# Performance work log

Hardware: AMD Instinct MI355X
Metric: run time of the kernel (lower is better)

## Reference

```python
import jax, jax.numpy as jnp
import numpy as np

DECAY = 0.99
EPSILON = 1e-05
CODEBOOK_SIZE = 1024
DIM = 128


def setup_inputs() -> dict:
    key = jax.random.key(0)
    k1, k2, k3, k4 = jax.random.split(key, 4)
    x = jax.random.normal(k1, (8, 8192, DIM), dtype=jnp.float32)
    embed = jax.random.normal(k2, (CODEBOOK_SIZE, DIM), dtype=jnp.float32)
    cluster_size = jax.random.uniform(k3, (CODEBOOK_SIZE,), dtype=jnp.float32)
    embed_avg = jax.random.normal(k4, (CODEBOOK_SIZE, DIM), dtype=jnp.float32)
    return {"x": x, "embed": embed, "cluster_size": cluster_size, "embed_avg": embed_avg}


def reference(x, embed, cluster_size, embed_avg):
    shape = x.shape
    flat = x.reshape(-1, shape[-1])  # [N, dim]

    # quantize: negative squared euclidean distance, argmax == nearest code
    dist = -(jnp.sum(flat * flat, axis=1, keepdims=True)
             - 2.0 * flat @ embed.T
             + jnp.sum(embed * embed, axis=1)[None, :])  # [N, K]
    embed_ind = jnp.argmax(dist, axis=-1)  # [N]

    quantize = embed[embed_ind].reshape(shape)            # dequantize
    embed_ind_out = embed_ind.reshape(shape[:-1])

    # training-time EMA updates (one-hot expressed as segment_sum)
    batch_cluster_size = jax.ops.segment_sum(
        jnp.ones_like(embed_ind, dtype=flat.dtype), embed_ind,
        num_segments=CODEBOOK_SIZE)                       # == one_hot.sum(0)
    new_cluster_size = cluster_size * DECAY + (1.0 - DECAY) * batch_cluster_size

    embed_sum = jax.ops.segment_sum(flat, embed_ind,
                                    num_segments=CODEBOOK_SIZE)  # == (x.T @ one_hot).T
    new_embed_avg = embed_avg * DECAY + (1.0 - DECAY) * embed_sum

    total = new_cluster_size.sum()
    smoothed = (new_cluster_size + EPSILON) / (total + CODEBOOK_SIZE * EPSILON)
    smoothed_counts = smoothed * total
    new_embed = new_embed_avg / smoothed_counts[:, None]

    return quantize, embed_ind_out, new_cluster_size, new_embed_avg, new_embed
```

## Files before the change

kernel.cpp:

```cpp
#include <hip/hip_runtime.h>
#include <math.h>

#define DIM 128
#define KCODES 1024
#define NROWS 65536

typedef short bf16x8 __attribute__((ext_vector_type(8)));
typedef float f32x4 __attribute__((ext_vector_type(4)));

#define WS_COUNTS 0
#define WS_ESUM   1024
#define WS_IOFF   132096
#define WS_TOTAL  133120
#define WS_ENORM2 133124
#define WS_EBF    134148
#define WS_WIN    461828
#define WS_SORTED 527364
#define WS_SCODE  592900

#define OFF_Q   0
#define OFF_IND 8388608
#define OFF_NCS 8454144
#define OFF_NEA 8455168
#define OFF_NE  8586240

#define LDST 136

static __device__ __forceinline__ unsigned short f2bf(float f) {
    unsigned u = __float_as_uint(f);
    unsigned r = (u + 0x7FFFu + ((u >> 16) & 1u)) >> 16;
    return (unsigned short)r;
}

__global__ __launch_bounds__(64) void k_prep(const float* __restrict__ embed,
                                             unsigned short* __restrict__ ebf,
                                             float* __restrict__ en2,
                                             float* __restrict__ counts,
                                             float* __restrict__ esum) {
    int k = blockIdx.x;
    int l = threadIdx.x;
    if (l == 0) counts[k] = 0.0f;
    *(float2*)&esum[(size_t)k * DIM + l * 2] = (float2){0.0f, 0.0f};
    float2 v = *(const float2*)&embed[(size_t)k * DIM + l * 2];
    ushort2 b;
    b.x = f2bf(v.x);
    b.y = f2bf(v.y);
    *(ushort2*)&ebf[k * DIM + l * 2] = b;
    float s = v.x * v.x + v.y * v.y;
    #pragma unroll
    for (int off = 32; off; off >>= 1) s += __shfl_xor(s, off);
    if (l == 0) en2[k] = 512.0f - 0.5f * s;
}

__global__ __launch_bounds__(256, 2) void k_fused(const float* __restrict__ x,
                                                  const float* __restrict__ embed,
                                                  const unsigned short* __restrict__ ebf,
                                                  const float* __restrict__ en2g,
                                                  int* __restrict__ win_g,
                                                  float* __restrict__ counts,
                                                  float* __restrict__ out) {
    __shared__ unsigned short xbuf[128 * LDST];
    __shared__ unsigned short ebuf[128 * LDST];
    __shared__ float en2s[KCODES];
    __shared__ int winS[128];

    const int tid = threadIdx.x;
    const int row0 = blockIdx.x * 128;

    #pragma unroll
    for (int i = 0; i < 4; ++i) en2s[i * 256 + tid] = en2g[i * 256 + tid];

    #pragma unroll
    for (int i = 0; i < 16; ++i) {
        int idx4 = i * 256 + tid;
        int lin = idx4 * 4;
        int r = lin >> 7, d = lin & 127;
        float4 v = *(const float4*)&x[(size_t)(row0 + r) * DIM + d];
        ushort4 b;
        b.x = f2bf(v.x); b.y = f2bf(v.y); b.z = f2bf(v.z); b.w = f2bf(v.w);
        *(ushort4*)&xbuf[r * LDST + d] = b;
    }

    const int lane = tid & 63;
    const int wv = tid >> 6;
    const int ch = wv & 1;
    const int rh = (wv >> 1) * 64;
    const int l15 = lane & 15;
    const int q = lane >> 4;

    float m1[4][4], m2[4][4];
    #pragma unroll
    for (int a = 0; a < 4; ++a)
        #pragma unroll
        for (int b = 0; b < 4; ++b) { m1[a][b] = 0.0f; m2[a][b] = 0.0f; }

    for (int ct = 0; ct < 8; ++ct) {
        const int c0 = ct * 128;
        __syncthreads();
        #pragma unroll
        for (int i = 0; i < 8; ++i) {
            int idx8 = i * 256 + tid;
            int r = idx8 >> 4;
            int d = (idx8 & 15) * 8;
            uint4 v = *(const uint4*)&ebf[(size_t)(c0 + r) * DIM + d];
            *(uint4*)&ebuf[r * LDST + d] = v;
        }
        __syncthreads();

        f32x4 acc[4][4];
        #pragma unroll
        for (int cl = 0; cl < 4; ++cl) {
            float en = en2s[c0 + ch * 64 + cl * 16 + l15];
            #pragma unroll
            for (int rt = 0; rt < 4; ++rt) acc[rt][cl] = (f32x4){en, en, en, en};
        }

        #pragma unroll
        for (int ks = 0; ks < 4; ++ks) {
            bf16x8 af[4], bf[4];
            #pragma unroll
            for (int t = 0; t < 4; ++t)
                af[t] = *(const bf16x8*)&xbuf[(rh + t * 16 + l15) * LDST + ks * 32 + q * 8];
            #pragma unroll
            for (int t = 0; t < 4; ++t)
                bf[t] = *(const bf16x8*)&ebuf[(ch * 64 + t * 16 + l15) * LDST + ks * 32 + q * 8];
            #pragma unroll
            for (int rt = 0; rt < 4; ++rt)
                #pragma unroll
                for (int cl = 0; cl < 4; ++cl)
                    acc[rt][cl] = __builtin_amdgcn_mfma_f32_16x16x32_bf16(af[rt], bf[cl],
                                                                          acc[rt][cl], 0, 0, 0);
        }

        #pragma unroll
        for (int cl = 0; cl < 4; ++cl) {
            unsigned cu = (unsigned)(c0 + ch * 64 + cl * 16 + l15);
            #pragma unroll
            for (int rt = 0; rt < 4; ++rt)
                #pragma unroll
                for (int rg = 0; rg < 4; ++rg) {
                    float s = acc[rt][cl][rg];
                    float kf = __uint_as_float((__float_as_uint(s) & ~1023u) | cu);
                    m2[rt][rg] = __builtin_amdgcn_fmed3f(m1[rt][rg], m2[rt][rg], kf);
                    m1[rt][rg] = fmaxf(m1[rt][rg], kf);
                }
        }
    }

    __syncthreads();
    float* scratch = (float*)xbuf;
    #pragma unroll
    for (int rt = 0; rt < 4; ++rt)
        #pragma unroll
        for (int rg = 0; rg < 4; ++rg) {
            float a1 = m1[rt][rg], a2 = m2[rt][rg];
            #pragma unroll
            for (int off = 1; off <= 8; off <<= 1) {
                float o1 = __shfl_xor(a1, off);
                float o2 = __shfl_xor(a2, off);
                float t = fmaxf(a2, o2);
                a2 = __builtin_amdgcn_fmed3f(a1, o1, t);
                a1 = fmaxf(a1, o1);
            }
            if (l15 == 0) {
                int row = rh + rt * 16 + q * 4 + rg;
                scratch[row * 4 + ch * 2 + 0] = a1;
                scratch[row * 4 + ch * 2 + 1] = a2;
            }
        }

    unsigned* hist = (unsigned*)ebuf;
    #pragma unroll
    for (int i = 0; i < 4; ++i) hist[i * 256 + tid] = 0u;
    __syncthreads();

    {
        const int sub = tid & 15;
        const int g = tid >> 4;
        #pragma unroll 2
        for (int rr = 0; rr < 8; ++rr) {
            const int lrow = g * 8 + rr;
            const float* sp = &scratch[lrow * 4];
            int ci[4];
            ci[0] = (int)(__float_as_uint(sp[0]) & 1023u);
            ci[1] = (int)(__float_as_uint(sp[1]) & 1023u);
            ci[2] = (int)(__float_as_uint(sp[2]) & 1023u);
            ci[3] = (int)(__float_as_uint(sp[3]) & 1023u);

            const float* xr = &x[(size_t)(row0 + lrow) * DIM + sub * 4];
            float4 xa = *(const float4*)xr;
            float4 xb = *(const float4*)(xr + 64);

            double d[4];
            #pragma unroll
            for (int j = 0; j < 4; ++j) {
                const float* er = &embed[(size_t)ci[j] * DIM + sub * 4];
                float4 ea4 = *(const float4*)er;
                float4 eb4 = *(const float4*)(er + 64);
                double t0 = (double)xa.x - (double)ea4.x;
                double t1 = (double)xa.y - (double)ea4.y;
                double t2 = (double)xa.z - (double)ea4.z;
                double t3 = (double)xa.w - (double)ea4.w;
                double t4 = (double)xb.x - (double)eb4.x;
                double t5 = (double)xb.y - (double)eb4.y;
                double t6 = (double)xb.z - (double)eb4.z;
                double t7 = (double)xb.w - (double)eb4.w;
                d[j] = ((t0 * t0 + t1 * t1) + (t2 * t2 + t3 * t3)) +
                       ((t4 * t4 + t5 * t5) + (t6 * t6 + t7 * t7));
            }
            #pragma unroll
            for (int off = 1; off <= 8; off <<= 1) {
                #pragma unroll
                for (int j = 0; j < 4; ++j) d[j] += __shfl_xor(d[j], off);
            }

            int win = ci[0];
            double dw = d[0];
            #pragma unroll
            for (int j = 1; j < 4; ++j) {
                bool b = (d[j] < dw) || (d[j] == dw && ci[j] < win);
                dw = b ? d[j] : dw;
                win = b ? ci[j] : win;
            }
            if (sub == 0) winS[lrow] = win;
        }
    }
    __syncthreads();

    if (tid < 128) {
        int w = winS[tid];
        atomicAdd(&hist[w], 1u);
        win_g[row0 + tid] = w;
        out[OFF_IND + row0 + tid] = (float)w;
    }

    #pragma unroll 4
    for (int i = 0; i < 32; ++i) {
        int lrow = wv * 32 + i;
        int w = winS[lrow];
        float2 v = *(const float2*)&embed[(size_t)w * DIM + lane * 2];
        *(float2*)&out[OFF_Q + (size_t)(row0 + lrow) * DIM + lane * 2] = v;
    }

    __syncthreads();
    #pragma unroll
    for (int i = 0; i < 4; ++i) {
        unsigned c = hist[i * 256 + tid];
        if (c) atomicAdd(&counts[i * 256 + tid], (float)c);
    }
}

__global__ __launch_bounds__(1024) void k_offsets(const float* __restrict__ cs,
                                                  float* __restrict__ out,
                                                  float* __restrict__ ws) {
    __shared__ int wsum[16];
    __shared__ float wtot[16];
    const float* counts = ws + WS_COUNTS;
    int* ioff = (int*)(ws + WS_IOFF);

    int t = threadIdx.x;
    int lane = t & 63, w = t >> 6;
    float cf = counts[t];
    int c = (int)cf;
    float ncs = cs[t] * 0.99f + 0.01f * cf;
    out[OFF_NCS + t] = ncs;

    int v = c;
    #pragma unroll
    for (int off = 1; off < 64; off <<= 1) {
        int o = __shfl_up(v, off);
        if (lane >= off) v += o;
    }
    float nf = ncs;
    #pragma unroll
    for (int off = 32; off; off >>= 1) nf += __shfl_xor(nf, off);

    if (lane == 63) wsum[w] = v;
    if (lane == 0) wtot[w] = nf;
    __syncthreads();

    int base = 0;
    for (int i = 0; i < w; ++i) base += wsum[i];
    ioff[t] = base + v - c;

    if (t == 0) {
        float tt = 0.f;
        for (int i = 0; i < 16; ++i) tt += wtot[i];
        ws[WS_TOTAL] = tt;
    }
}

__global__ __launch_bounds__(256) void k_sortscatter(const int* __restrict__ win_arr,
                                                     int* __restrict__ ioff,
                                                     int* __restrict__ sorted,
                                                     int* __restrict__ scode) {
    int row = blockIdx.x * 256 + threadIdx.x;
    int w = win_arr[row];
    int pos = atomicAdd(&ioff[w], 1);
    sorted[pos] = row;
    scode[pos] = w;
}

__global__ __launch_bounds__(256) void k_segsum(const float* __restrict__ x,
                                                const int* __restrict__ sorted,
                                                const int* __restrict__ scode,
                                                float* __restrict__ esum) {
    const int lane = threadIdx.x & 63;
    const int wv = threadIdx.x >> 6;
    const int base = blockIdx.x * 64 + wv * 16;

    int p = base + (lane & 15);
    int srow = sorted[p];
    int sc = scode[p];

    float ax = 0.f, ay = 0.f;
    int cur = __shfl(sc, 0);

    #pragma unroll
    for (int j = 0; j < 16; ++j) {
        int row = __shfl(srow, j);
        int c = __shfl(sc, j);
        if (c != cur) {
            atomicAdd(&esum[cur * DIM + lane * 2], ax);
            atomicAdd(&esum[cur * DIM + lane * 2 + 1], ay);
            ax = 0.f; ay = 0.f;
            cur = c;
        }
        float2 v = *(const float2*)&x[(size_t)row * DIM + lane * 2];
        ax += v.x;
        ay += v.y;
    }
    atomicAdd(&esum[cur * DIM + lane * 2], ax);
    atomicAdd(&esum[cur * DIM + lane * 2 + 1], ay);
}

__global__ __launch_bounds__(256) void k_embed(const float* __restrict__ ea,
                                               const float* __restrict__ ws,
                                               float* __restrict__ out) {
    int i = blockIdx.x * 256 + threadIdx.x;
    int k = i >> 7;
    float nea = ea[i] * 0.99f + 0.01f * ws[WS_ESUM + i];
    out[OFF_NEA + i] = nea;
    float total = ws[WS_TOTAL];
    float ncs = out[OFF_NCS + k];
    float sm = (ncs + 1e-5f) / (total + 1024.0f * 1e-5f);
    out[OFF_NE + i] = nea / (sm * total);
}

extern "C" void kernel_launch(void* const* d_in, const int* in_sizes, int n_in,
                              void* d_out, int out_size, void* d_ws, size_t ws_size,
                              hipStream_t stream) {
    const float* x     = (const float*)d_in[0];
    const float* embed = (const float*)d_in[1];
    const float* cs    = (const float*)d_in[2];
    const float* ea    = (const float*)d_in[3];
    float* out = (float*)d_out;
    float* ws  = (float*)d_ws;

    k_prep<<<KCODES, 64, 0, stream>>>(embed, (unsigned short*)(ws + WS_EBF),
                                      ws + WS_ENORM2, ws + WS_COUNTS, ws + WS_ESUM);
    k_fused<<<NROWS / 128, 256, 0, stream>>>(x, embed,
                                             (const unsigned short*)(ws + WS_EBF),
                                             ws + WS_ENORM2, (int*)(ws + WS_WIN),
                                             ws + WS_COUNTS, out);
    k_offsets<<<1, 1024, 0, stream>>>(cs, out, ws);
    k_sortscatter<<<NROWS / 256, 256, 0, stream>>>((const int*)(ws + WS_WIN),
                                                   (int*)(ws + WS_IOFF),
                                                   (int*)(ws + WS_SORTED),
                                                   (int*)(ws + WS_SCODE));
    k_segsum<<<1024, 256, 0, stream>>>(x, (const int*)(ws + WS_SORTED),
                                       (const int*)(ws + WS_SCODE), ws + WS_ESUM);
    k_embed<<<131072 / 256, 256, 0, stream>>>(ea, ws, out);
}
```

Before: 184.0 us.

## Keep x fragments in registers and share one LDS buffer for higher occupancy

The x tile's bf16 MFMA A-fragments are now loaded once into registers before the codebook loop, so xbuf and ebuf merge into a single shared buffer that roughly halves LDS per block. The accumulator is split into two 32-code halves to hold register pressure down, and launch bounds rise from 2 to 3 blocks per SIMD. The intent is more resident waves to hide memory and LDS latency. The costs are 64 extra VGPRs for A fragments under a tighter register budget, with a risk of spills, and the scratch and histogram regions now overlap one buffer at fixed offsets.

```diff
diff --git a/kernel.cpp b/kernel.cpp
--- a/kernel.cpp
+++ b/kernel.cpp
@@ -52,15 +52,14 @@
     if (l == 0) en2[k] = 512.0f - 0.5f * s;
 }
 
-__global__ __launch_bounds__(256, 2) void k_fused(const float* __restrict__ x,
+__global__ __launch_bounds__(256, 3) void k_fused(const float* __restrict__ x,
                                                   const float* __restrict__ embed,
                                                   const unsigned short* __restrict__ ebf,
                                                   const float* __restrict__ en2g,
                                                   int* __restrict__ win_g,
                                                   float* __restrict__ counts,
                                                   float* __restrict__ out) {
-    __shared__ unsigned short xbuf[128 * LDST];
-    __shared__ unsigned short ebuf[128 * LDST];
+    __shared__ unsigned short buf[128 * LDST];
     __shared__ float en2s[KCODES];
     __shared__ int winS[128];
 
@@ -78,8 +77,9 @@
         float4 v = *(const float4*)&x[(size_t)(row0 + r) * DIM + d];
         ushort4 b;
         b.x = f2bf(v.x); b.y = f2bf(v.y); b.z = f2bf(v.z); b.w = f2bf(v.w);
-        *(ushort4*)&xbuf[r * LDST + d] = b;
-    }
+        *(ushort4*)&buf[r * LDST + d] = b;
+    }
+    __syncthreads();
 
     const int lane = tid & 63;
     const int wv = tid >> 6;
@@ -88,6 +88,14 @@
     const int l15 = lane & 15;
     const int q = lane >> 4;
 
+    bf16x8 af[4][4];
+    #pragma unroll
+    for (int ks = 0; ks < 4; ++ks)
+        #pragma unroll
+        for (int t = 0; t < 4; ++t)
+            af[ks][t] = *(const bf16x8*)&buf[(rh + t * 16 + l15) * LDST + ks * 32 + q * 8];
+    __syncthreads();
+
     float m1[4][4], m2[4][4];
     #pragma unroll
     for (int a = 0; a < 4; ++a)
@@ -96,59 +104,61 @@
 
     for (int ct = 0; ct < 8; ++ct) {
         const int c0 = ct * 128;
-        __syncthreads();
         #pragma unroll
         for (int i = 0; i < 8; ++i) {
             int idx8 = i * 256 + tid;
             int r = idx8 >> 4;
             int d = (idx8 & 15) * 8;
             uint4 v = *(const uint4*)&ebf[(size_t)(c0 + r) * DIM + d];
-            *(uint4*)&ebuf[r * LDST + d] = v;
+            *(uint4*)&buf[r * LDST + d] = v;
         }
         __syncthreads();
 
-        f32x4 acc[4][4];
-        #pragma unroll
-        for (int cl = 0; cl < 4; ++cl) {
-            float en = en2s[c0 + ch * 64 + cl * 16 + l15];
-            #pragma unroll
-            for (int rt = 0; rt < 4; ++rt) acc[rt][cl] = (f32x4){en, en, en, en};
-        }
-
-        #pragma unroll
-        for (int ks = 0; ks < 4; ++ks) {
-            bf16x8 af[4], bf[4];
-            #pragma unroll
-            for (int t = 0; t < 4; ++t)
-                af[t] = *(const bf16x8*)&xbuf[(rh + t * 16 + l15) * LDST + ks * 32 + q * 8];
-            #pragma unroll
-            for (int t = 0; t < 4; ++t)
-                bf[t] = *(const bf16x8*)&ebuf[(ch * 64 + t * 16 + l15) * LDST + ks * 32 + q * 8];
-            #pragma unroll
-            for (int rt = 0; rt < 4; ++rt)
-                #pragma unroll
-                for (int cl = 0; cl < 4; ++cl)
-                    acc[rt][cl] = __builtin_amdgcn_mfma_f32_16x16x32_bf16(af[rt], bf[cl],
-                                                                          acc[rt][cl], 0, 0, 0);
-        }
-
-        #pragma unroll
-        for (int cl = 0; cl < 4; ++cl) {
-            unsigned cu = (unsigned)(c0 + ch * 64 + cl * 16 + l15);
-            #pragma unroll
-            for (int rt = 0; rt < 4; ++rt)
-                #pragma unroll
-                for (int rg = 0; rg < 4; ++rg) {
-                    float s = acc[rt][cl][rg];
-                    float kf = __uint_as_float((__float_as_uint(s) & ~1023u) | cu);
-                    m2[rt][rg] = __builtin_amdgcn_fmed3f(m1[rt][rg], m2[rt][rg], kf);
-                    m1[rt][rg] = fmaxf(m1[rt][rg], kf);
-                }
-        }
-    }
-
-    __syncthreads();
-    float* scratch = (float*)xbuf;
+        #pragma unroll
+        for (int clh = 0; clh < 2; ++clh) {
+            f32x4 acc[4][2];
+            #pragma unroll
+            for (int c2 = 0; c2 < 2; ++c2) {
+                float en = en2s[c0 + ch * 64 + clh * 32 + c2 * 16 + l15];
+                #pragma unroll
+                for (int rt = 0; rt < 4; ++rt) acc[rt][c2] = (f32x4){en, en, en, en};
+            }
+
+            #pragma unroll
+            for (int ks = 0; ks < 4; ++ks) {
+                bf16x8 bfr[2];
+                #pragma unroll
+                for (int c2 = 0; c2 < 2; ++c2)
+                    bfr[c2] = *(const bf16x8*)&buf[(ch * 64 + clh * 32 + c2 * 16 + l15) * LDST +
+                                                   ks * 32 + q * 8];
+                #pragma unroll
+                for (int rt = 0; rt < 4; ++rt)
+                    #pragma unroll
+                    for (int c2 = 0; c2 < 2; ++c2)
+                        acc[rt][c2] = __builtin_amdgcn_mfma_f32_16x16x32_bf16(af[ks][rt], bfr[c2],
+                                                                              acc[rt][c2], 0, 0, 0);
+            }
+
+            #pragma unroll
+            for (int c2 = 0; c2 < 2; ++c2) {
+                unsigned cu = (unsigned)(c0 + ch * 64 + clh * 32 + c2 * 16 + l15);
+                #pragma unroll
+                for (int rt = 0; rt < 4; ++rt)
+                    #pragma unroll
+                    for (int rg = 0; rg < 4; ++rg) {
+                        float s = acc[rt][c2][rg];
+                        float kf = __uint_as_float((__float_as_uint(s) & ~1023u) | cu);
+                        m2[rt][rg] = __builtin_amdgcn_fmed3f(m1[rt][rg], m2[rt][rg], kf);
+                        m1[rt][rg] = fmaxf(m1[rt][rg], kf);
+                    }
+            }
+        }
+        __syncthreads();
+    }
+
+    float* scratch = (float*)buf;
+    unsigned* hist = (unsigned*)buf + 512;
+
     #pragma unroll
     for (int rt = 0; rt < 4; ++rt)
         #pragma unroll
@@ -169,7 +179,6 @@
             }
         }
 
-    unsigned* hist = (unsigned*)ebuf;
     #pragma unroll
     for (int i = 0; i < 4; ++i) hist[i * 256 + tid] = 0u;
     __syncthreads();
```

Result: slower. 205.1 us (+11.5%).

## Double-buffer codebook tiles and widen fused kernel to 512 threads

Applied to the files above, without the earlier changes.

The fused distance/argmax kernel now runs 8 waves per block instead of 4, giving each wave 32 rows instead of 64. X fragments are kept in registers across all codebook tiles, and codebook tiles are double-buffered in LDS, with the next tile prefetched into registers while the current one is processed, so each tile needs one barrier instead of two. The goal is to hide global-load latency and raise occupancy. In exchange, every wave reloads the codebook B fragments for half as many MFMAs, and register pressure rises from the held A fragments.

```diff
diff --git a/kernel.cpp b/kernel.cpp
--- a/kernel.cpp
+++ b/kernel.cpp
@@ -52,15 +52,14 @@
     if (l == 0) en2[k] = 512.0f - 0.5f * s;
 }
 
-__global__ __launch_bounds__(256, 2) void k_fused(const float* __restrict__ x,
+__global__ __launch_bounds__(512, 4) void k_fused(const float* __restrict__ x,
                                                   const float* __restrict__ embed,
                                                   const unsigned short* __restrict__ ebf,
                                                   const float* __restrict__ en2g,
                                                   int* __restrict__ win_g,
                                                   float* __restrict__ counts,
                                                   float* __restrict__ out) {
-    __shared__ unsigned short xbuf[128 * LDST];
-    __shared__ unsigned short ebuf[128 * LDST];
+    __shared__ unsigned short buf[2][128 * LDST];
     __shared__ float en2s[KCODES];
     __shared__ int winS[128];
 
@@ -68,67 +67,90 @@
     const int row0 = blockIdx.x * 128;
 
     #pragma unroll
-    for (int i = 0; i < 4; ++i) en2s[i * 256 + tid] = en2g[i * 256 + tid];
-
-    #pragma unroll
-    for (int i = 0; i < 16; ++i) {
-        int idx4 = i * 256 + tid;
+    for (int i = 0; i < 2; ++i) en2s[i * 512 + tid] = en2g[i * 512 + tid];
+
+    #pragma unroll
+    for (int i = 0; i < 8; ++i) {
+        int idx4 = i * 512 + tid;
         int lin = idx4 * 4;
         int r = lin >> 7, d = lin & 127;
         float4 v = *(const float4*)&x[(size_t)(row0 + r) * DIM + d];
         ushort4 b;
         b.x = f2bf(v.x); b.y = f2bf(v.y); b.z = f2bf(v.z); b.w = f2bf(v.w);
-        *(ushort4*)&xbuf[r * LDST + d] = b;
-    }
+        *(ushort4*)&buf[0][r * LDST + d] = b;
+    }
+    __syncthreads();
 
     const int lane = tid & 63;
     const int wv = tid >> 6;
     const int ch = wv & 1;
-    const int rh = (wv >> 1) * 64;
+    const int rh = (wv >> 1) * 32;
     const int l15 = lane & 15;
     const int q = lane >> 4;
 
-    float m1[4][4], m2[4][4];
-    #pragma unroll
-    for (int a = 0; a < 4; ++a)
+    bf16x8 af[4][2];
+    #pragma unroll
+    for (int ks = 0; ks < 4; ++ks)
+        #pragma unroll
+        for (int t = 0; t < 2; ++t)
+            af[ks][t] = *(const bf16x8*)&buf[0][(rh + t * 16 + l15) * LDST + ks * 32 + q * 8];
+
+    uint4 er[4];
+    #pragma unroll
+    for (int i = 0; i < 4; ++i) {
+        int idx8 = i * 512 + tid;
+        int r = idx8 >> 4;
+        int d = (idx8 & 15) * 8;
+        er[i] = *(const uint4*)&ebf[(size_t)r * DIM + d];
+    }
+    #pragma unroll
+    for (int i = 0; i < 4; ++i) {
+        int idx8 = i * 512 + tid;
+        int r = idx8 >> 4;
+        int d = (idx8 & 15) * 8;
+        *(uint4*)&buf[1][r * LDST + d] = er[i];
+    }
+    __syncthreads();
+
+    float m1[2][4], m2[2][4];
+    #pragma unroll
+    for (int a = 0; a < 2; ++a)
         #pragma unroll
         for (int b = 0; b < 4; ++b) { m1[a][b] = 0.0f; m2[a][b] = 0.0f; }
 
     for (int ct = 0; ct < 8; ++ct) {
         const int c0 = ct * 128;
-        __syncthreads();
-        #pragma unroll
-        for (int i = 0; i < 8; ++i) {
-            int idx8 = i * 256 + tid;
-            int r = idx8 >> 4;
-            int d = (idx8 & 15) * 8;
-            uint4 v = *(const uint4*)&ebf[(size_t)(c0 + r) * DIM + d];
-            *(uint4*)&ebuf[r * LDST + d] = v;
-        }
-        __syncthreads();
-
-        f32x4 acc[4][4];
+        const unsigned short* cbuf = buf[1 ^ (ct & 1)];
+
+        if (ct < 7) {
+            #pragma unroll
+            for (int i = 0; i < 4; ++i) {
+                int idx8 = i * 512 + tid;
+                int r = idx8 >> 4;
+                int d = (idx8 & 15) * 8;
+                er[i] = *(const uint4*)&ebf[(size_t)(c0 + 128 + r) * DIM + d];
+            }
+        }
+
+        f32x4 acc[2][4];
         #pragma unroll
         for (int cl = 0; cl < 4; ++cl) {
             float en = en2s[c0 + ch * 64 + cl * 16 + l15];
             #pragma unroll
-            for (int rt = 0; rt < 4; ++rt) acc[rt][cl] = (f32x4){en, en, en, en};
+            for (int rt = 0; rt < 2; ++rt) acc[rt][cl] = (f32x4){en, en, en, en};
         }
 
         #pragma unroll
         for (int ks = 0; ks < 4; ++ks) {
-            bf16x8 af[4], bf[4];
-            #pragma unroll
-            for (int t = 0; t < 4; ++t)
-                af[t] = *(const bf16x8*)&xbuf[(rh + t * 16 + l15) * LDST + ks * 32 + q * 8];
-            #pragma unroll
-            for (int t = 0; t < 4; ++t)
-                bf[t] = *(const bf16x8*)&ebuf[(ch * 64 + t * 16 + l15) * LDST + ks * 32 + q * 8];
-            #pragma unroll
-            for (int rt = 0; rt < 4; ++rt)
+            bf16x8 bfr[4];
+            #pragma unroll
+            for (int cl = 0; cl < 4; ++cl)
+                bfr[cl] = *(const bf16x8*)&cbuf[(ch * 64 + cl * 16 + l15) * LDST + ks * 32 + q * 8];
+            #pragma unroll
+            for (int rt = 0; rt < 2; ++rt)
                 #pragma unroll
                 for (int cl = 0; cl < 4; ++cl)
-                    acc[rt][cl] = __builtin_amdgcn_mfma_f32_16x16x32_bf16(af[rt], bf[cl],
+                    acc[rt][cl] = __builtin_amdgcn_mfma_f32_16x16x32_bf16(af[ks][rt], bfr[cl],
                                                                           acc[rt][cl], 0, 0, 0);
         }
 
@@ -136,7 +158,7 @@
         for (int cl = 0; cl < 4; ++cl) {
             unsigned cu = (unsigned)(c0 + ch * 64 + cl * 16 + l15);
             #pragma unroll
-            for (int rt = 0; rt < 4; ++rt)
+            for (int rt = 0; rt < 2; ++rt)
                 #pragma unroll
                 for (int rg = 0; rg < 4; ++rg) {
                     float s = acc[rt][cl][rg];
@@ -145,12 +167,25 @@
                     m1[rt][rg] = fmaxf(m1[rt][rg], kf);
                 }
         }
-    }
-
-    __syncthreads();
-    float* scratch = (float*)xbuf;
-    #pragma unroll
-    for (int rt = 0; rt < 4; ++rt)
+
+        if (ct < 7) {
+            unsigned short* nbuf = buf[ct & 1];
+            #pragma unroll
+            for (int i = 0; i < 4; ++i) {
+                int idx8 = i * 512 + tid;
+                int r = idx8 >> 4;
+                int d = (idx8 & 15) * 8;
+                *(uint4*)&nbuf[r * LDST + d] = er[i];
+            }
+        }
+        __syncthreads();
+    }
+
+    float* scratch = (float*)buf[0];
+    unsigned* hist = (unsigned*)buf[0] + 512;
+
+    #pragma unroll
+    for (int rt = 0; rt < 2; ++rt)
         #pragma unroll
         for (int rg = 0; rg < 4; ++rg) {
             float a1 = m1[rt][rg], a2 = m2[rt][rg];
@@ -169,17 +204,16 @@
             }
         }
 
-    unsigned* hist = (unsigned*)ebuf;
-    #pragma unroll
-    for (int i = 0; i < 4; ++i) hist[i * 256 + tid] = 0u;
+    #pragma unroll
+    for (int i = 0; i < 2; ++i) hist[i * 512 + tid] = 0u;
     __syncthreads();
 
     {
         const int sub = tid & 15;
         const int g = tid >> 4;
         #pragma unroll 2
-        for (int rr = 0; rr < 8; ++rr) {
-            const int lrow = g * 8 + rr;
+        for (int rr = 0; rr < 4; ++rr) {
+            const int lrow = g * 4 + rr;
             const float* sp = &scratch[lrow * 4];
             int ci[4];
             ci[0] = (int)(__float_as_uint(sp[0]) & 1023u);
@@ -194,9 +228,9 @@
             double d[4];
             #pragma unroll
             for (int j = 0; j < 4; ++j) {
-                const float* er = &embed[(size_t)ci[j] * DIM + sub * 4];
-                float4 ea4 = *(const float4*)er;
-                float4 eb4 = *(const float4*)(er + 64);
+                const float* er2 = &embed[(size_t)ci[j] * DIM + sub * 4];
+                float4 ea4 = *(const float4*)er2;
+                float4 eb4 = *(const float4*)(er2 + 64);
                 double t0 = (double)xa.x - (double)ea4.x;
                 double t1 = (double)xa.y - (double)ea4.y;
                 double t2 = (double)xa.z - (double)ea4.z;
@@ -235,8 +269,8 @@
     }
 
     #pragma unroll 4
-    for (int i = 0; i < 32; ++i) {
-        int lrow = wv * 32 + i;
+    for (int i = 0; i < 16; ++i) {
+        int lrow = wv * 16 + i;
         int w = winS[lrow];
         float2 v = *(const float2*)&embed[(size_t)w * DIM + lane * 2];
         *(float2*)&out[OFF_Q + (size_t)(row0 + lrow) * DIM + lane * 2] = v;
@@ -244,9 +278,9 @@
 
     __syncthreads();
     #pragma unroll
-    for (int i = 0; i < 4; ++i) {
-        unsigned c = hist[i * 256 + tid];
-        if (c) atomicAdd(&counts[i * 256 + tid], (float)c);
+    for (int i = 0; i < 2; ++i) {
+        unsigned c = hist[i * 512 + tid];
+        if (c) atomicAdd(&counts[i * 512 + tid], (float)c);
     }
 }
 
@@ -359,7 +393,7 @@
 
     k_prep<<<KCODES, 64, 0, stream>>>(embed, (unsigned short*)(ws + WS_EBF),
                                       ws + WS_ENORM2, ws + WS_COUNTS, ws + WS_ESUM);
-    k_fused<<<NROWS / 128, 256, 0, stream>>>(x, embed,
+    k_fused<<<NROWS / 128, 512, 0, stream>>>(x, embed,
                                              (const unsigned short*)(ws + WS_EBF),
                                              ws + WS_ENORM2, (int*)(ws + WS_WIN),
                                              ws + WS_COUNTS, out);
```

After: 186.7 us. No clear change (+1.5%).
